# Performance work log

Measured on AMD Instinct MI355X. Metric: run time of the kernel, lower is better.

Reference implementation:

```python
import jax, jax.numpy as jnp
import numpy as np

B, NS, D, H, L, NQ, NK = 32, 4096, 256, 4, 6, 512, 1024
DH = D // H
SCALE = 1.0 / np.sqrt(DH)


def _ln(x, scale, bias, eps=1e-5):
    m = jnp.mean(x, axis=-1, keepdims=True)
    v = jnp.mean((x - m) ** 2, axis=-1, keepdims=True)
    return (x - m) * jax.lax.rsqrt(v + eps) * scale + bias


def setup_inputs() -> dict:
    key = jax.random.key(0)
    ks = jax.random.split(key, 12)
    d = {
        'update_tensor': jax.random.normal(ks[0], (B, NS, D), jnp.float32) * 0.1,
        'emb_table': jax.random.normal(ks[1], (NS + 1, D), jnp.float32) * 0.1,
        'mask_logits': jax.random.uniform(ks[2], (L, NQ, NK), jnp.float32),
        'Wq': jax.random.normal(ks[3], (D, D), jnp.float32) * 0.05,
        'Wk': jax.random.normal(ks[4], (D, D), jnp.float32) * 0.05,
        'Wv': jax.random.normal(ks[5], (D, D), jnp.float32) * 0.05,
        'Wo': jax.random.normal(ks[6], (D, D), jnp.float32) * 0.05,
        'W1': jax.random.normal(ks[7], (D, D), jnp.float32) * 0.05,
        'b1': jnp.zeros((D,), jnp.float32),
        'W2': jax.random.normal(ks[8], (D, D), jnp.float32) * 0.05,
        'b2': jnp.zeros((D,), jnp.float32),
        'sys_scale': jnp.ones((D,), jnp.float32),
        'sys_bias': jnp.zeros((D,), jnp.float32),
        'eff_scale': jnp.ones((D,), jnp.float32),
        'eff_bias': jnp.zeros((D,), jnp.float32),
        'inner_scale': jnp.ones((D,), jnp.float32),
        'inner_bias': jnp.zeros((D,), jnp.float32),
        'outer_scale': jnp.ones((D,), jnp.float32),
        'outer_bias': jnp.zeros((D,), jnp.float32),
        'query_idx': jax.random.randint(ks[9], (L, NQ), 0, NS).astype(jnp.int32),
        'key_idx': jax.random.randint(ks[10], (L, NK), 0, NS).astype(jnp.int32),
    }
    return d


def _hitr(q, k, mask, Wq, Wk, Wv, Wo, W1, b1, W2, b2, in_s, in_b, out_s, out_b):
    # q: [B,NQ,D] (pre-normed), k: [B,NK,D], mask: [NQ,NK] bool
    Q = jnp.einsum('bqd,de->bqe', q, Wq).reshape(B, NQ, H, DH)
    K = jnp.einsum('bkd,de->bke', k, Wk).reshape(B, NK, H, DH)
    V = jnp.einsum('bkd,de->bke', k, Wv).reshape(B, NK, H, DH)
    scores = jnp.einsum('bqhd,bkhd->bhqk', Q, K) * SCALE
    scores = jnp.where(mask[None, None], scores, jnp.float32(-1e9))
    attn = jax.nn.softmax(scores, axis=-1)
    ctx = jnp.einsum('bhqk,bkhd->bqhd', attn, V).reshape(B, NQ, D)
    h = _ln(jnp.einsum('bqd,de->bqe', ctx, Wo), in_s, in_b)
    ffn = jnp.einsum('bqd,de->bqe', jax.nn.gelu(jnp.einsum('bqd,de->bqe', h, W1) + b1), W2) + b2
    return _ln(h + ffn, out_s, out_b)


def reference(update_tensor, emb_table, mask_logits, Wq, Wk, Wv, Wo, W1, b1, W2, b2,
              sys_scale, sys_bias, eff_scale, eff_bias, inner_scale, inner_bias,
              outer_scale, outer_bias, query_idx, key_idx):
    update_result = jnp.zeros_like(update_tensor)
    for l in range(L):  # static hierarchy levels
        qi, ki = query_idx[l], key_idx[l]
        mask = mask_logits[l] > 0.5
        q = _ln(emb_table[qi][None] + update_tensor[:, qi], sys_scale, sys_bias)
        k = _ln(emb_table[ki][None] + update_tensor[:, ki], sys_scale, sys_bias)
        res = _ln(_hitr(q, k, mask, Wq, Wk, Wv, Wo, W1, b1, W2, b2,
                        inner_scale, inner_bias, outer_scale, outer_bias),
                  eff_scale, eff_bias)
        update_tensor = update_tensor.at[:, qi].add(res)
        update_result = update_result.at[:, qi].add(res)
    return update_result
```

## Files before the change

kernel.cpp:

```cpp
#include <hip/hip_runtime.h>
#include <cstdint>
#include <cstddef>

#define B_ 32
#define NS_ 4096
#define D_ 256
#define H_ 4
#define L_ 6
#define NQ_ 512
#define NK_ 1024
#define DH_ 64
#define SCALE_ 0.125f

typedef unsigned short ushort_t;
typedef unsigned long long u64_t;
typedef __bf16 bf16x8 __attribute__((ext_vector_type(8)));
typedef float f32x4 __attribute__((ext_vector_type(4)));

__device__ __forceinline__ ushort_t f2bf(float f) {
  unsigned u = __float_as_uint(f);
  u += 0x7fffu + ((u >> 16) & 1u);
  return (ushort_t)(u >> 16);
}

__device__ __forceinline__ void gld16(const void* g, void* l) {
  __builtin_amdgcn_global_load_lds(
      (__attribute__((address_space(1))) void*)(uintptr_t)g,
      (__attribute__((address_space(3))) void*)(uintptr_t)l, 16, 0, 0);
}

__device__ __forceinline__ float2 block_sum2(float a, float b) {
  __shared__ float sA[4], sB[4];
#pragma unroll
  for (int o = 32; o; o >>= 1) {
    a += __shfl_xor(a, o);
    b += __shfl_xor(b, o);
  }
  const int w = threadIdx.x >> 6;
  __syncthreads();
  if ((threadIdx.x & 63) == 0) { sA[w] = a; sB[w] = b; }
  __syncthreads();
  return make_float2(sA[0] + sA[1] + sA[2] + sA[3], sB[0] + sB[1] + sB[2] + sB[3]);
}

__global__ __launch_bounds__(256) void prep_w(
    const float* __restrict__ w0, const float* __restrict__ w1,
    const float* __restrict__ w2, const float* __restrict__ w3,
    const float* __restrict__ w4, const float* __restrict__ w5,
    ushort_t* __restrict__ wt) {
  const int sel = blockIdx.x >> 8;
  const int n = blockIdx.x & 255;
  const int k = threadIdx.x;
  const float* W = sel == 0 ? w0 : sel == 1 ? w1 : sel == 2 ? w2
                 : sel == 3 ? w3 : sel == 4 ? w4 : w5;
  wt[sel * 65536 + n * 256 + k] = f2bf(W[k * 256 + n]);
}

__global__ __launch_bounds__(256) void prep_mask(
    const float* __restrict__ ml, u64_t* __restrict__ mb) {
  const long gid = (long)blockIdx.x * 256 + threadIdx.x;
  const bool m = ml[gid] > 0.5f;
  const u64_t bal = __ballot(m);
  if ((threadIdx.x & 63) == 0) mb[gid >> 6] = bal;
}

__global__ __launch_bounds__(256) void gather_ln(
    const float* __restrict__ ut, const float* __restrict__ emb,
    const int* __restrict__ qidx, const int* __restrict__ kidx,
    const float* __restrict__ sc, const float* __restrict__ bi,
    ushort_t* __restrict__ qn, ushort_t* __restrict__ kn) {
  const int r = blockIdx.x;
  const int t = threadIdx.x;
  int bb, idx;
  ushort_t* dst;
  long drow;
  if (r < B_ * NQ_) {
    bb = r >> 9; idx = qidx[r & (NQ_ - 1)]; dst = qn; drow = r;
  } else {
    const int r2 = r - B_ * NQ_;
    bb = r2 >> 10; idx = kidx[r2 & (NK_ - 1)]; dst = kn; drow = r2;
  }
  const float x = emb[(long)idx * 256 + t] + ut[((long)bb * NS_ + idx) * 256 + t];
  const float2 s = block_sum2(x, x * x);
  const float mean = s.x * (1.f / 256.f);
  const float var = s.y * (1.f / 256.f) - mean * mean;
  const float inv = rsqrtf(var + 1e-5f);
  dst[drow * 256 + t] = f2bf((x - mean) * inv * sc[t] + bi[t]);
}

template <int EPI>
__device__ __forceinline__ void gemm_body(
    const ushort_t* __restrict__ A, const ushort_t* __restrict__ Bt,
    void* __restrict__ Cout, long m0, int n0, ushort_t* lAB) {
  ushort_t* lA = lAB;
  ushort_t* lB = lAB + 8192;
  const int tid = threadIdx.x;
  const int lane = tid & 63, w = tid >> 6;
  const int quad = lane >> 4, l16 = lane & 15;
  const int wm = w & 1, wn = w >> 1;

  f32x4 acc[4][4] = {};

  for (int kt = 0; kt < 4; ++kt) {
    const int k0 = kt * 64;
#pragma unroll
    for (int p = 0; p < 4; ++p) {
      const int ob = p * 4096 + tid * 16;
      const int row = ob >> 7;
      const int chunk = ((ob >> 4) & 7) ^ (row & 7);
      gld16(A + (m0 + row) * 256 + k0 + chunk * 8, (char*)lA + p * 4096 + w * 1024);
      gld16(Bt + (long)(n0 + row) * 256 + k0 + chunk * 8, (char*)lB + p * 4096 + w * 1024);
    }
    __syncthreads();
#pragma unroll
    for (int ki = 0; ki < 2; ++ki) {
      bf16x8 af[4], bfr[4];
#pragma unroll
      for (int i = 0; i < 4; ++i) {
        const int ra = wm * 64 + i * 16 + l16;
        const int ca = (ki * 4 + quad) ^ (ra & 7);
        af[i] = *(const bf16x8*)&lA[ra * 64 + ca * 8];
        const int rb = wn * 64 + i * 16 + l16;
        const int cb = (ki * 4 + quad) ^ (rb & 7);
        bfr[i] = *(const bf16x8*)&lB[rb * 64 + cb * 8];
      }
#pragma unroll
      for (int mi = 0; mi < 4; ++mi)
#pragma unroll
        for (int ni = 0; ni < 4; ++ni)
          acc[mi][ni] = __builtin_amdgcn_mfma_f32_16x16x32_bf16(af[mi], bfr[ni], acc[mi][ni], 0, 0, 0);
    }
    __syncthreads();
  }

  if (EPI == 4) {
    const long b = m0 >> 10;
    const int kvseg = (int)(m0 & 1023);
#pragma unroll
    for (int hg = 0; hg < 2; ++hg) {
      if (wn == hg) {
#pragma unroll
        for (int mi = 0; mi < 4; ++mi)
#pragma unroll
          for (int ni = 0; ni < 4; ++ni)
#pragma unroll
            for (int r = 0; r < 4; ++r) {
              const int dh = ni * 16 + l16;
              const int kvl = wm * 64 + mi * 16 + quad * 4 + r;
              lAB[dh * 128 + (((kvl >> 3) ^ (dh & 15)) << 3) + (kvl & 7)] =
                  f2bf(acc[mi][ni][r]);
            }
      }
      __syncthreads();
      {
        const int dh = tid >> 2;
        const int head = (n0 >> 6) + hg;
        ushort_t* dst = (ushort_t*)Cout +
            ((b * 4 + head) * 64 + dh) * 1024 + kvseg;
#pragma unroll
        for (int i = 0; i < 4; ++i) {
          const int c = (tid & 3) * 4 + i;
          const int cs = c ^ (dh & 15);
          *(uint4*)(dst + c * 8) = *(const uint4*)&lAB[dh * 128 + cs * 8];
        }
      }
      __syncthreads();
    }
    return;
  }

#pragma unroll
  for (int mi = 0; mi < 4; ++mi) {
#pragma unroll
    for (int ni = 0; ni < 4; ++ni) {
#pragma unroll
      for (int r = 0; r < 4; ++r) {
        const long row = m0 + wm * 64 + mi * 16 + quad * 4 + r;
        const int col = n0 + wn * 64 + ni * 16 + l16;
        float v = acc[mi][ni][r];
        if (EPI == 5) v *= SCALE_;
        ((ushort_t*)Cout)[row * 256 + col] = f2bf(v);
      }
    }
  }
}

__global__ __launch_bounds__(256) void gemm_qkv(
    const ushort_t* __restrict__ qn, const ushort_t* __restrict__ kn,
    const ushort_t* __restrict__ wt,
    ushort_t* __restrict__ Qb, ushort_t* __restrict__ Kb, ushort_t* __restrict__ Vt) {
  __shared__ ushort_t lAB[16384];
  int idx = blockIdx.x;
  if (idx < 256) {
    gemm_body<5>(qn, wt, Qb, (long)(idx & 127) * 128, (idx >> 7) * 128, lAB);
  } else if (idx < 768) {
    idx -= 256;
    gemm_body<0>(kn, wt + 65536, Kb, (long)(idx & 255) * 128, (idx >> 8) * 128, lAB);
  } else {
    idx -= 768;
    gemm_body<4>(kn, wt + 131072, Vt, (long)(idx & 255) * 128, (idx >> 8) * 128, lAB);
  }
}

template <int MODE>
__global__ __launch_bounds__(256) void gemm_band(
    const ushort_t* __restrict__ A, const ushort_t* __restrict__ Bt,
    const float* __restrict__ bias,
    const float* __restrict__ ln1s, const float* __restrict__ ln1b,
    const float* __restrict__ ln2s, const float* __restrict__ ln2b,
    const float* __restrict__ hfres, const int* __restrict__ qidx,
    float* __restrict__ outF, ushort_t* __restrict__ outB,
    float* __restrict__ ut, float* __restrict__ out) {
  __shared__ ushort_t lA[4096];
  __shared__ ushort_t lB[16384];
  __shared__ float sS1[64][4], sS2[64][4];
  const int tid = threadIdx.x;
  const int lane = tid & 63, w = tid >> 6;
  const int quad = lane >> 4, l16 = lane & 15;
  const long m0 = (long)blockIdx.x * 64;

  f32x4 acc[4][4] = {};

  for (int kt = 0; kt < 4; ++kt) {
    const int k0 = kt * 64;
#pragma unroll
    for (int p = 0; p < 2; ++p) {
      const int ob = p * 4096 + tid * 16;
      const int row = ob >> 7;
      const int chunk = ((ob >> 4) & 7) ^ (row & 7);
      gld16(A + (m0 + row) * 256 + k0 + chunk * 8, (char*)lA + p * 4096 + w * 1024);
    }
#pragma unroll
    for (int p = 0; p < 8; ++p) {
      const int ob = p * 4096 + tid * 16;
      const int row = ob >> 7;
      const int chunk = ((ob >> 4) & 7) ^ (row & 7);
      gld16(Bt + (long)row * 256 + k0 + chunk * 8, (char*)lB + p * 4096 + w * 1024);
    }
    __syncthreads();
#pragma unroll
    for (int ki = 0; ki < 2; ++ki) {
      bf16x8 af[4], bfr[4];
#pragma unroll
      for (int i = 0; i < 4; ++i) {
        const int ra = i * 16 + l16;
        const int ca = (ki * 4 + quad) ^ (ra & 7);
        af[i] = *(const bf16x8*)&lA[ra * 64 + ca * 8];
        const int rb = w * 64 + i * 16 + l16;
        const int cb = (ki * 4 + quad) ^ (rb & 7);
        bfr[i] = *(const bf16x8*)&lB[rb * 64 + cb * 8];
      }
#pragma unroll
      for (int mi = 0; mi < 4; ++mi)
#pragma unroll
        for (int ni = 0; ni < 4; ++ni)
          acc[mi][ni] = __builtin_amdgcn_mfma_f32_16x16x32_bf16(af[mi], bfr[ni], acc[mi][ni], 0, 0, 0);
    }
    __syncthreads();
  }

  if (MODE == 2) {
    float bcol[4];
#pragma unroll
    for (int ni = 0; ni < 4; ++ni) bcol[ni] = bias[w * 64 + ni * 16 + l16];
#pragma unroll
    for (int mi = 0; mi < 4; ++mi)
#pragma unroll
      for (int r = 0; r < 4; ++r) {
        const long row = m0 + mi * 16 + quad * 4 + r;
#pragma unroll
        for (int ni = 0; ni < 4; ++ni) {
          float v = acc[mi][ni][r] + bcol[ni];
          const float u = 0.7978845608028654f * (v + 0.044715f * v * v * v);
          v = 0.5f * v * (1.0f + tanhf(u));
          outB[row * 256 + (w * 64 + ni * 16 + l16)] = f2bf(v);
        }
      }
    return;
  }

  if (MODE == 6) {
#pragma unroll
    for (int mi = 0; mi < 4; ++mi)
#pragma unroll
      for (int r = 0; r < 4; ++r) {
        float a1 = 0.f, a2 = 0.f;
#pragma unroll
        for (int ni = 0; ni < 4; ++ni) {
          const float v = acc[mi][ni][r];
          a1 += v; a2 += v * v;
        }
#pragma unroll
        for (int off = 1; off < 16; off <<= 1) {
          a1 += __shfl_xor(a1, off);
          a2 += __shfl_xor(a2, off);
        }
        if (l16 == 0) {
          sS1[mi * 16 + quad * 4 + r][w] = a1;
          sS2[mi * 16 + quad * 4 + r][w] = a2;
        }
      }
    __syncthreads();
    float l1sv[4], l1bv[4];
#pragma unroll
    for (int ni = 0; ni < 4; ++ni) {
      const int col = w * 64 + ni * 16 + l16;
      l1sv[ni] = ln1s[col]; l1bv[ni] = ln1b[col];
    }
#pragma unroll
    for (int mi = 0; mi < 4; ++mi)
#pragma unroll
      for (int r = 0; r < 4; ++r) {
        const int rowi = mi * 16 + quad * 4 + r;
        const f32x4 v1 = *(const f32x4*)&sS1[rowi][0];
        const f32x4 v2 = *(const f32x4*)&sS2[rowi][0];
        const float s1 = v1[0] + v1[1] + v1[2] + v1[3];
        const float s2 = v2[0] + v2[1] + v2[2] + v2[3];
        const float mean = s1 * (1.f / 256.f);
        const float inv = rsqrtf(s2 * (1.f / 256.f) - mean * mean + 1e-5f);
        const long row = m0 + rowi;
#pragma unroll
        for (int ni = 0; ni < 4; ++ni) {
          const int col = w * 64 + ni * 16 + l16;
          const float y = (acc[mi][ni][r] - mean) * inv * l1sv[ni] + l1bv[ni];
          outF[row * 256 + col] = y;
          outB[row * 256 + col] = f2bf(y);
        }
      }
    return;
  }

  {
    float bcol[4], l1sv[4], l1bv[4], l2sv[4], l2bv[4];
#pragma unroll
    for (int ni = 0; ni < 4; ++ni) {
      const int col = w * 64 + ni * 16 + l16;
      bcol[ni] = bias[col];
      l1sv[ni] = ln1s[col]; l1bv[ni] = ln1b[col];
      l2sv[ni] = ln2s[col]; l2bv[ni] = ln2b[col];
    }
#pragma unroll
    for (int mi = 0; mi < 4; ++mi)
#pragma unroll
      for (int r = 0; r < 4; ++r) {
        const long row = m0 + mi * 16 + quad * 4 + r;
        float a1 = 0.f, a2 = 0.f;
#pragma unroll
        for (int ni = 0; ni < 4; ++ni) {
          const int col = w * 64 + ni * 16 + l16;
          const float v = acc[mi][ni][r] + bcol[ni] + hfres[row * 256 + col];
          acc[mi][ni][r] = v;
          a1 += v; a2 += v * v;
        }
#pragma unroll
        for (int off = 1; off < 16; off <<= 1) {
          a1 += __shfl_xor(a1, off);
          a2 += __shfl_xor(a2, off);
        }
        if (l16 == 0) {
          sS1[mi * 16 + quad * 4 + r][w] = a1;
          sS2[mi * 16 + quad * 4 + r][w] = a2;
        }
      }
    __syncthreads();
    float py1[4][4], py2[4][4];
#pragma unroll
    for (int mi = 0; mi < 4; ++mi)
#pragma unroll
      for (int r = 0; r < 4; ++r) {
        const int rowi = mi * 16 + quad * 4 + r;
        const f32x4 v1 = *(const f32x4*)&sS1[rowi][0];
        const f32x4 v2 = *(const f32x4*)&sS2[rowi][0];
        const float s1 = v1[0] + v1[1] + v1[2] + v1[3];
        const float s2 = v2[0] + v2[1] + v2[2] + v2[3];
        const float mean = s1 * (1.f / 256.f);
        const float inv = rsqrtf(s2 * (1.f / 256.f) - mean * mean + 1e-5f);
        float a1 = 0.f, a2 = 0.f;
#pragma unroll
        for (int ni = 0; ni < 4; ++ni) {
          const float y = (acc[mi][ni][r] - mean) * inv * l1sv[ni] + l1bv[ni];
          acc[mi][ni][r] = y;
          a1 += y; a2 += y * y;
        }
        py1[mi][r] = a1; py2[mi][r] = a2;
      }
    __syncthreads();
#pragma unroll
    for (int mi = 0; mi < 4; ++mi)
#pragma unroll
      for (int r = 0; r < 4; ++r) {
        float a1 = py1[mi][r], a2 = py2[mi][r];
#pragma unroll
        for (int off = 1; off < 16; off <<= 1) {
          a1 += __shfl_xor(a1, off);
          a2 += __shfl_xor(a2, off);
        }
        if (l16 == 0) {
          sS1[mi * 16 + quad * 4 + r][w] = a1;
          sS2[mi * 16 + quad * 4 + r][w] = a2;
        }
      }
    __syncthreads();
#pragma unroll
    for (int mi = 0; mi < 4; ++mi)
#pragma unroll
      for (int r = 0; r < 4; ++r) {
        const int rowi = mi * 16 + quad * 4 + r;
        const f32x4 v1 = *(const f32x4*)&sS1[rowi][0];
        const f32x4 v2 = *(const f32x4*)&sS2[rowi][0];
        const float s1 = v1[0] + v1[1] + v1[2] + v1[3];
        const float s2 = v2[0] + v2[1] + v2[2] + v2[3];
        const float mean = s1 * (1.f / 256.f);
        const float inv = rsqrtf(s2 * (1.f / 256.f) - mean * mean + 1e-5f);
        const long row = m0 + rowi;
        const int idx = qidx[(int)(row & (NQ_ - 1))];
        const long base = ((row >> 9) * (long)NS_ + idx) * 256;
#pragma unroll
        for (int ni = 0; ni < 4; ++ni) {
          const int col = w * 64 + ni * 16 + l16;
          const float z = (acc[mi][ni][r] - mean) * inv * l2sv[ni] + l2bv[ni];
          atomicAdd(&ut[base + col], z);
          atomicAdd(&out[base + col], z);
        }
      }
  }
}

__global__ __launch_bounds__(256) void attn_kernel(
    const ushort_t* __restrict__ Qb, const ushort_t* __restrict__ Kb,
    const ushort_t* __restrict__ Vt, const u64_t* __restrict__ mbits,
    ushort_t* __restrict__ ctx) {
  __shared__ ushort_t lQ[4096], lK[4096], lVt[4096], lP[4096];
  const int tid = threadIdx.x;
  const int lane = tid & 63, w = tid >> 6;
  const int quad = lane >> 4, l16 = lane & 15;
  const int bid = blockIdx.x;
  const int qt = bid >> 7, pair = bid & 127;
  const int h = pair & 3, b = pair >> 2;
  const int q0 = qt * 64;
  const long qrow0 = (long)b * NQ_ + q0;
  const long krow0 = (long)b * NK_;
  const ushort_t* vbase = Vt + ((long)pair * 64) * 1024;
  const u64_t* mrow = mbits + (long)(q0 + w * 16 + quad * 4) * (NK_ / 64);

#pragma unroll
  for (int p = 0; p < 2; ++p) {
    const int ob = p * 4096 + tid * 16;
    const int row = ob >> 7;
    const int chunk = ((ob >> 4) & 7) ^ (row & 7);
    gld16(Qb + (qrow0 + row) * 256 + h * 64 + chunk * 8, (char*)lQ + p * 4096 + w * 1024);
    gld16(Kb + (krow0 + row) * 256 + h * 64 + chunk * 8, (char*)lK + p * 4096 + w * 1024);
  }

  f32x4 o_acc[4] = {};
  f32x4 l_acc = {};
  bf16x8 ones;
#pragma unroll
  for (int i = 0; i < 8; ++i) ones[i] = (__bf16)1.0f;

  u64_t wd[4];
#pragma unroll
  for (int r = 0; r < 4; ++r) wd[r] = mrow[r << 4];

  for (int kt = 0; kt < 16; ++kt) {
    __syncthreads();

#pragma unroll
    for (int p = 0; p < 2; ++p) {
      const int ob = p * 4096 + tid * 16;
      const int row = ob >> 7;
      const int chunk = ((ob >> 4) & 7) ^ (row & 7);
      gld16(vbase + (long)row * 1024 + kt * 64 + chunk * 8,
            (char*)lVt + p * 4096 + w * 1024);
    }

    f32x4 s[4] = {};
    __builtin_amdgcn_s_setprio(1);
#pragma unroll
    for (int ki = 0; ki < 2; ++ki) {
      const int rq = w * 16 + l16;
      const int cq = (ki * 4 + quad) ^ (rq & 7);
      const bf16x8 qf = *(const bf16x8*)&lQ[rq * 64 + cq * 8];
#pragma unroll
      for (int ni = 0; ni < 4; ++ni) {
        const int rk = ni * 16 + l16;
        const int ck = (ki * 4 + quad) ^ (rk & 7);
        const bf16x8 kf = *(const bf16x8*)&lK[rk * 64 + ck * 8];
        s[ni] = __builtin_amdgcn_mfma_f32_16x16x32_bf16(qf, kf, s[ni], 0, 0, 0);
      }
    }
    __builtin_amdgcn_s_setprio(0);

    u64_t wdn[4];
    if (kt < 15) {
#pragma unroll
      for (int r = 0; r < 4; ++r) wdn[r] = mrow[(r << 4) + kt + 1];
    }

#pragma unroll
    for (int r = 0; r < 4; ++r) {
      const int rowp = w * 16 + quad * 4 + r;
#pragma unroll
      for (int ni = 0; ni < 4; ++ni) {
        const bool keep = (wd[r] >> (ni * 16 + l16)) & 1ull;
        const float pv = keep ? __expf(s[ni][r]) : 0.f;
        const int col = ni * 16 + l16;
        lP[rowp * 64 + (((col >> 3) ^ (rowp & 7)) << 3) + (col & 7)] = f2bf(pv);
      }
    }
    if (kt < 15) {
#pragma unroll
      for (int r = 0; r < 4; ++r) wd[r] = wdn[r];
    }

    __syncthreads();

    if (kt < 15) {
#pragma unroll
      for (int p = 0; p < 2; ++p) {
        const int ob = p * 4096 + tid * 16;
        const int row = ob >> 7;
        const int chunk = ((ob >> 4) & 7) ^ (row & 7);
        gld16(Kb + (krow0 + (kt + 1) * 64 + row) * 256 + h * 64 + chunk * 8,
              (char*)lK + p * 4096 + w * 1024);
      }
    }

    __builtin_amdgcn_s_setprio(1);
#pragma unroll
    for (int ki = 0; ki < 2; ++ki) {
      const int rp = w * 16 + l16;
      const int cp = (ki * 4 + quad) ^ (rp & 7);
      const bf16x8 pf = *(const bf16x8*)&lP[rp * 64 + cp * 8];
      l_acc = __builtin_amdgcn_mfma_f32_16x16x32_bf16(pf, ones, l_acc, 0, 0, 0);
#pragma unroll
      for (int ni = 0; ni < 4; ++ni) {
        const int rv = ni * 16 + l16;
        const int cv = (ki * 4 + quad) ^ (rv & 7);
        const bf16x8 vf = *(const bf16x8*)&lVt[rv * 64 + cv * 8];
        o_acc[ni] = __builtin_amdgcn_mfma_f32_16x16x32_bf16(pf, vf, o_acc[ni], 0, 0, 0);
      }
    }
    __builtin_amdgcn_s_setprio(0);
  }

#pragma unroll
  for (int r = 0; r < 4; ++r) {
    const float inv = 1.0f / l_acc[r];
    const long rowg = qrow0 + w * 16 + quad * 4 + r;
#pragma unroll
    for (int ni = 0; ni < 4; ++ni) {
      const int col = h * 64 + ni * 16 + l16;
      ctx[rowg * 256 + col] = f2bf(o_acc[ni][r] * inv);
    }
  }
}

extern "C" void kernel_launch(void* const* d_in, const int* in_sizes, int n_in,
                              void* d_out, int out_size, void* d_ws, size_t ws_size,
                              hipStream_t stream) {
  float* ut = (float*)d_in[0];
  const float* emb = (const float*)d_in[1];
  const float* maskl = (const float*)d_in[2];
  const float* Wq = (const float*)d_in[3];
  const float* Wk = (const float*)d_in[4];
  const float* Wv = (const float*)d_in[5];
  const float* Wo = (const float*)d_in[6];
  const float* W1 = (const float*)d_in[7];
  const float* b1 = (const float*)d_in[8];
  const float* W2 = (const float*)d_in[9];
  const float* b2 = (const float*)d_in[10];
  const float* sys_s = (const float*)d_in[11];
  const float* sys_b = (const float*)d_in[12];
  const float* eff_s = (const float*)d_in[13];
  const float* eff_b = (const float*)d_in[14];
  const float* in_s = (const float*)d_in[15];
  const float* in_b = (const float*)d_in[16];
  const float* out_s = (const float*)d_in[17];
  const float* out_b = (const float*)d_in[18];
  const int* qidx = (const int*)d_in[19];
  const int* kidx = (const int*)d_in[20];
  float* out = (float*)d_out;

  char* p = (char*)d_ws;
  auto carve = [&](size_t bytes) {
    void* r = (void*)p;
    p += (bytes + 255) & ~(size_t)255;
    return r;
  };
  ushort_t* wt = (ushort_t*)carve((size_t)6 * 65536 * 2);
  u64_t* mb = (u64_t*)carve((size_t)L_ * NQ_ * (NK_ / 64) * 8);
  ushort_t* qn = (ushort_t*)carve((size_t)16384 * 256 * 2);
  ushort_t* kn = (ushort_t*)carve((size_t)32768 * 256 * 2);
  ushort_t* Qb = (ushort_t*)carve((size_t)16384 * 256 * 2);
  ushort_t* Kb = (ushort_t*)carve((size_t)32768 * 256 * 2);
  ushort_t* Vt = (ushort_t*)carve((size_t)32768 * 256 * 2);

  ushort_t* ctx = qn;
  ushort_t* g = Qb;
  ushort_t* hb = Kb;
  float* hf = (float*)Vt;

  hipMemsetAsync(d_out, 0, (size_t)out_size, stream);
  prep_w<<<1536, 256, 0, stream>>>(Wq, Wk, Wv, Wo, W1, W2, wt);
  prep_mask<<<(L_ * NQ_ * NK_) / 256, 256, 0, stream>>>(maskl, mb);

  for (int l = 0; l < L_; ++l) {
    gather_ln<<<B_ * (NQ_ + NK_), 256, 0, stream>>>(
        ut, emb, qidx + l * NQ_, kidx + l * NK_, sys_s, sys_b, qn, kn);
    gemm_qkv<<<1280, 256, 0, stream>>>(qn, kn, wt, Qb, Kb, Vt);
    attn_kernel<<<1024, 256, 0, stream>>>(
        Qb, Kb, Vt, mb + (size_t)l * NQ_ * (NK_ / 64), ctx);
    gemm_band<6><<<256, 256, 0, stream>>>(
        ctx, wt + 3 * 65536, nullptr, in_s, in_b, nullptr, nullptr,
        nullptr, nullptr, hf, hb, nullptr, nullptr);
    gemm_band<2><<<256, 256, 0, stream>>>(
        hb, wt + 4 * 65536, b1, nullptr, nullptr, nullptr, nullptr,
        nullptr, nullptr, nullptr, g, nullptr, nullptr);
    gemm_band<7><<<256, 256, 0, stream>>>(
        g, wt + 5 * 65536, b2, out_s, out_b, eff_s, eff_b,
        hf, qidx + l * NQ_, nullptr, nullptr, ut, out);
  }
}
```

Before: 1.391 ms.

## Triple-buffer gemm_band K-loop and use wave-per-row gather layernorm

gemm_band now splits K into eight 32-wide tiles in a three-deep LDS ring. Explicit vmcnt waits let global-to-LDS loads for tile k+2 overlap the MFMA work on tile k, where before each 64-wide tile was loaded and then synchronized. gather_ln now handles one row per wave with float4 loads and a pure shuffle reduction, removing the block-level shared-memory reduction and its two __syncthreads. The hand-tuned vmcnt counts depend on the exact number of loads each stage issues and are fragile if the stage changes.

```diff
diff --git a/kernel.cpp b/kernel.cpp
--- a/kernel.cpp
+++ b/kernel.cpp
@@ -27,20 +27,6 @@
   __builtin_amdgcn_global_load_lds(
       (__attribute__((address_space(1))) void*)(uintptr_t)g,
       (__attribute__((address_space(3))) void*)(uintptr_t)l, 16, 0, 0);
-}
-
-__device__ __forceinline__ float2 block_sum2(float a, float b) {
-  __shared__ float sA[4], sB[4];
-#pragma unroll
-  for (int o = 32; o; o >>= 1) {
-    a += __shfl_xor(a, o);
-    b += __shfl_xor(b, o);
-  }
-  const int w = threadIdx.x >> 6;
-  __syncthreads();
-  if ((threadIdx.x & 63) == 0) { sA[w] = a; sB[w] = b; }
-  __syncthreads();
-  return make_float2(sA[0] + sA[1] + sA[2] + sA[3], sB[0] + sB[1] + sB[2] + sB[3]);
 }
 
 __global__ __launch_bounds__(256) void prep_w(
@@ -69,23 +55,38 @@
     const int* __restrict__ qidx, const int* __restrict__ kidx,
     const float* __restrict__ sc, const float* __restrict__ bi,
     ushort_t* __restrict__ qn, ushort_t* __restrict__ kn) {
-  const int r = blockIdx.x;
-  const int t = threadIdx.x;
+  const int w = threadIdx.x >> 6, lane = threadIdx.x & 63;
+  const int R = blockIdx.x * 4 + w;
   int bb, idx;
   ushort_t* dst;
   long drow;
-  if (r < B_ * NQ_) {
-    bb = r >> 9; idx = qidx[r & (NQ_ - 1)]; dst = qn; drow = r;
+  if (R < B_ * NQ_) {
+    bb = R >> 9; idx = qidx[R & (NQ_ - 1)]; dst = qn; drow = R;
   } else {
-    const int r2 = r - B_ * NQ_;
+    const int r2 = R - B_ * NQ_;
     bb = r2 >> 10; idx = kidx[r2 & (NK_ - 1)]; dst = kn; drow = r2;
   }
-  const float x = emb[(long)idx * 256 + t] + ut[((long)bb * NS_ + idx) * 256 + t];
-  const float2 s = block_sum2(x, x * x);
-  const float mean = s.x * (1.f / 256.f);
-  const float var = s.y * (1.f / 256.f) - mean * mean;
-  const float inv = rsqrtf(var + 1e-5f);
-  dst[drow * 256 + t] = f2bf((x - mean) * inv * sc[t] + bi[t]);
+  const int c0 = lane * 4;
+  const float4 e = *(const float4*)(emb + (long)idx * 256 + c0);
+  const float4 u = *(const float4*)(ut + ((long)bb * NS_ + idx) * 256 + c0);
+  float x0 = e.x + u.x, x1 = e.y + u.y, x2 = e.z + u.z, x3 = e.w + u.w;
+  float s1 = x0 + x1 + x2 + x3;
+  float s2 = x0 * x0 + x1 * x1 + x2 * x2 + x3 * x3;
+#pragma unroll
+  for (int off = 1; off < 64; off <<= 1) {
+    s1 += __shfl_xor(s1, off);
+    s2 += __shfl_xor(s2, off);
+  }
+  const float mean = s1 * (1.f / 256.f);
+  const float inv = rsqrtf(s2 * (1.f / 256.f) - mean * mean + 1e-5f);
+  const float4 scv = *(const float4*)(sc + c0);
+  const float4 biv = *(const float4*)(bi + c0);
+  ushort4 o;
+  o.x = f2bf((x0 - mean) * inv * scv.x + biv.x);
+  o.y = f2bf((x1 - mean) * inv * scv.y + biv.y);
+  o.z = f2bf((x2 - mean) * inv * scv.z + biv.z);
+  o.w = f2bf((x3 - mean) * inv * scv.w + biv.w);
+  *(ushort4*)(dst + drow * 256 + c0) = o;
 }
 
 template <int EPI>
@@ -211,52 +212,60 @@
     const float* __restrict__ hfres, const int* __restrict__ qidx,
     float* __restrict__ outF, ushort_t* __restrict__ outB,
     float* __restrict__ ut, float* __restrict__ out) {
-  __shared__ ushort_t lA[4096];
-  __shared__ ushort_t lB[16384];
+  __shared__ ushort_t lA[3][2048];
+  __shared__ ushort_t lB[3][8192];
   __shared__ float sS1[64][4], sS2[64][4];
   const int tid = threadIdx.x;
   const int lane = tid & 63, w = tid >> 6;
   const int quad = lane >> 4, l16 = lane & 15;
   const long m0 = (long)blockIdx.x * 64;
 
+  auto stage = [&](int kt, int bu) {
+    const int k0 = kt * 32;
+    {
+      const int ob = tid * 16;
+      const int row = ob >> 6;
+      const int c = (ob >> 4) & 3;
+      gld16(A + (m0 + row) * 256 + k0 + (c ^ ((row >> 1) & 3)) * 8,
+            (char*)&lA[bu][0] + w * 1024);
+    }
+#pragma unroll
+    for (int p = 0; p < 4; ++p) {
+      const int ob = p * 4096 + tid * 16;
+      const int row = ob >> 6;
+      const int c = (ob >> 4) & 3;
+      gld16(Bt + (long)row * 256 + k0 + (c ^ ((row >> 1) & 3)) * 8,
+            (char*)&lB[bu][0] + p * 4096 + w * 1024);
+    }
+  };
+
   f32x4 acc[4][4] = {};
-
-  for (int kt = 0; kt < 4; ++kt) {
-    const int k0 = kt * 64;
-#pragma unroll
-    for (int p = 0; p < 2; ++p) {
-      const int ob = p * 4096 + tid * 16;
-      const int row = ob >> 7;
-      const int chunk = ((ob >> 4) & 7) ^ (row & 7);
-      gld16(A + (m0 + row) * 256 + k0 + chunk * 8, (char*)lA + p * 4096 + w * 1024);
-    }
-#pragma unroll
-    for (int p = 0; p < 8; ++p) {
-      const int ob = p * 4096 + tid * 16;
-      const int row = ob >> 7;
-      const int chunk = ((ob >> 4) & 7) ^ (row & 7);
-      gld16(Bt + (long)row * 256 + k0 + chunk * 8, (char*)lB + p * 4096 + w * 1024);
-    }
-    __syncthreads();
-#pragma unroll
-    for (int ki = 0; ki < 2; ++ki) {
-      bf16x8 af[4], bfr[4];
-#pragma unroll
-      for (int i = 0; i < 4; ++i) {
-        const int ra = i * 16 + l16;
-        const int ca = (ki * 4 + quad) ^ (ra & 7);
-        af[i] = *(const bf16x8*)&lA[ra * 64 + ca * 8];
-        const int rb = w * 64 + i * 16 + l16;
-        const int cb = (ki * 4 + quad) ^ (rb & 7);
-        bfr[i] = *(const bf16x8*)&lB[rb * 64 + cb * 8];
-      }
-#pragma unroll
-      for (int mi = 0; mi < 4; ++mi)
-#pragma unroll
-        for (int ni = 0; ni < 4; ++ni)
-          acc[mi][ni] = __builtin_amdgcn_mfma_f32_16x16x32_bf16(af[mi], bfr[ni], acc[mi][ni], 0, 0, 0);
-    }
-    __syncthreads();
+  stage(0, 0);
+  stage(1, 1);
+#pragma unroll
+  for (int kt = 0; kt < 8; ++kt) {
+    const int bu = kt % 3;
+    if (kt < 6) stage(kt + 2, (kt + 2) % 3);
+    if (kt < 6)       asm volatile("s_waitcnt vmcnt(10)" ::: "memory");
+    else if (kt == 6) asm volatile("s_waitcnt vmcnt(5)" ::: "memory");
+    else              asm volatile("s_waitcnt vmcnt(0)" ::: "memory");
+    __builtin_amdgcn_s_barrier();
+    __builtin_amdgcn_sched_barrier(0);
+    bf16x8 af[4], bfr[4];
+#pragma unroll
+    for (int i = 0; i < 4; ++i) {
+      const int ra = i * 16 + l16;
+      af[i] = *(const bf16x8*)&lA[bu][ra * 32 + ((quad ^ ((ra >> 1) & 3)) * 8)];
+      const int rb = w * 64 + i * 16 + l16;
+      bfr[i] = *(const bf16x8*)&lB[bu][rb * 32 + ((quad ^ ((rb >> 1) & 3)) * 8)];
+    }
+#pragma unroll
+    for (int mi = 0; mi < 4; ++mi)
+#pragma unroll
+      for (int ni = 0; ni < 4; ++ni)
+        acc[mi][ni] = __builtin_amdgcn_mfma_f32_16x16x32_bf16(af[mi], bfr[ni], acc[mi][ni], 0, 0, 0);
+    __builtin_amdgcn_sched_barrier(0);
+    __builtin_amdgcn_s_barrier();
   }
 
   if (MODE == 2) {
@@ -606,7 +615,7 @@
   prep_mask<<<(L_ * NQ_ * NK_) / 256, 256, 0, stream>>>(maskl, mb);
 
   for (int l = 0; l < L_; ++l) {
-    gather_ln<<<B_ * (NQ_ + NK_), 256, 0, stream>>>(
+    gather_ln<<<B_ * (NQ_ + NK_) / 4, 256, 0, stream>>>(
         ut, emb, qidx + l * NQ_, kidx + l * NK_, sys_s, sys_b, qn, kn);
     gemm_qkv<<<1280, 256, 0, stream>>>(qn, kn, wt, Qb, Kb, Vt);
     attn_kernel<<<1024, 256, 0, stream>>>(
```

After: 1.261 ms. 9.3% less time.
